# Kernel optimization log

Measured on AMD Instinct MI355X. Metric: run time of the kernel, lower is better.

The kernel has to match this reference:

```python
import jax, jax.numpy as jnp
import numpy as np

B_SZ = 8
D_MODEL = 512
D_STATE = 64
N2 = D_STATE // 2  # S4D uses complex-conjugate pairs -> d_state//2 complex modes
L_SEQ = 2048


def setup_inputs() -> dict:
    key = jax.random.key(0)
    ks = jax.random.split(key, 16)
    d = D_MODEL
    scale = 1.0 / np.sqrt(d)
    inp = {
        "x": jax.random.normal(ks[0], (B_SZ, d, L_SEQ), dtype=jnp.float32),
        # q/k/v projections (nn.Linear: weight (out,in), bias (out,))
        "Wq": jax.random.normal(ks[1], (d, d), dtype=jnp.float32) * scale,
        "bq": jax.random.normal(ks[2], (d,), dtype=jnp.float32) * scale,
        "Wk": jax.random.normal(ks[3], (d, d), dtype=jnp.float32) * scale,
        "bk": jax.random.normal(ks[4], (d,), dtype=jnp.float32) * scale,
        "Wv": jax.random.normal(ks[5], (d, d), dtype=jnp.float32) * scale,
        "bv": jax.random.normal(ks[6], (d,), dtype=jnp.float32) * scale,
        # Shift layer params
        "shift_C": jax.random.normal(ks[7], (1, d, D_STATE), dtype=jnp.float32),
        "shift_D": jax.random.normal(ks[8], (d,), dtype=jnp.float32),
        # S4D (diagonal SSM) params
        "log_dt": jax.random.uniform(ks[9], (d,), dtype=jnp.float32,
                                      minval=np.log(1e-3), maxval=np.log(1e-1)),
        "A_real": jnp.log(0.5 * jnp.ones((d, N2), dtype=jnp.float32)),
        "A_imag": jnp.broadcast_to(np.pi * jnp.arange(N2, dtype=jnp.float32), (d, N2)),
        "C_re": jax.random.normal(ks[10], (d, N2), dtype=jnp.float32) * np.sqrt(0.5),
        "C_im": jax.random.normal(ks[11], (d, N2), dtype=jnp.float32) * np.sqrt(0.5),
        "s4_D": jax.random.normal(ks[12], (d,), dtype=jnp.float32),
    }
    return inp


def _linear_chan(x, W, b):
    # x: (B, H, L); Linear applied over channel dim H -> (B, H_out, L)
    return jnp.einsum("bhl,dh->bdl", x, W) + b[:, None]


def _shift(u, C, Dp):
    """Shift SSM: causal conv with kernel = first L taps of C (computed via FFT
    exactly as the torch source does). u: (B, H, L)."""
    L = u.shape[-1]
    n = 2 * L
    H, S = C.shape[1], C.shape[2]
    Bmat = jnp.zeros((H, S), dtype=u.dtype).at[:, 0].set(1.0)
    B_fc = jnp.conj(jnp.fft.rfft(Bmat, n=n, axis=-1))  # (H, L+1)
    C_f = jnp.fft.rfft(C, n=n, axis=-1)                # (1, H, L+1)
    kernel = jnp.fft.irfft(B_fc * C_f, n=n, axis=-1)[..., :L]  # (1, H, L)
    kernel_f = jnp.fft.rfft(kernel, n=n, axis=-1)      # (1, H, L+1)
    u_f = jnp.fft.rfft(u, n=n, axis=-1)                # (B, H, L+1)
    y = jnp.fft.irfft(u_f * kernel_f, n=n, axis=-1)[..., :L]
    return y + u * Dp[:, None]


def _s4d(u, log_dt, A_real, A_imag, C_re, C_im, Dp):
    """Standard S4D forward: ZOH-discretized diagonal SSM kernel + FFT conv.
    u: (B, H, L)."""
    L = u.shape[-1]
    n = 2 * L
    dt = jnp.exp(log_dt)[:, None]                  # (H, 1)
    A = -jnp.exp(A_real) + 1j * A_imag             # (H, N2)
    dtA = A * dt                                   # (H, N2)
    C = (C_re + 1j * C_im) * (jnp.exp(dtA) - 1.0) / A
    vand = jnp.exp(dtA[:, :, None] * jnp.arange(L))  # (H, N2, L)
    K = 2.0 * jnp.einsum("hn,hnl->hl", C, vand).real  # (H, L)
    y = jnp.fft.irfft(jnp.fft.rfft(u, n=n, axis=-1) * jnp.fft.rfft(K, n=n, axis=-1),
                      n=n, axis=-1)[..., :L]
    return y + u * Dp[:, None]


def reference(x, Wq, bq, Wk, bk, Wv, bv, shift_C, shift_D,
              log_dt, A_real, A_imag, C_re, C_im, s4_D):
    q = _linear_chan(x, Wq, bq)
    k = _linear_chan(x, Wk, bk)
    v = _linear_chan(x, Wv, bv)
    shift_out = _shift(k, shift_C, shift_D)
    s4d_out = _s4d(v * shift_out, log_dt, A_real, A_imag, C_re, C_im, s4_D)
    return q * s4d_out
```

## Files before the change

### kernel.cpp

```cpp
#include <hip/hip_runtime.h>
#include <cstdint>


#define DMODEL 512
#define LSEQ 2048

typedef _Float16 half_t;
typedef __attribute__((ext_vector_type(4))) _Float16 half4v;
typedef __attribute__((ext_vector_type(8))) _Float16 half8v;
typedef __attribute__((ext_vector_type(4))) float floatx4;

#define SW(R, c) ((R) * 64 + ((((c) >> 3) ^ ((R) & 7)) << 3) + ((c) & 7))

__device__ __forceinline__ void gload_lds16(const half_t* g, half_t* l) {
  __builtin_amdgcn_global_load_lds(
      (const __attribute__((address_space(1))) uint32_t*)g,
      (__attribute__((address_space(3))) uint32_t*)l, 16, 0, 0);
}

#define WAIT_LGKM_BAR()                                   \
  do {                                                    \
    asm volatile("s_waitcnt lgkmcnt(0)" ::: "memory");    \
    __builtin_amdgcn_s_barrier();                         \
    __builtin_amdgcn_sched_barrier(0);                    \
  } while (0)

__global__ __launch_bounds__(256) void prep(
    const float* __restrict__ x, const float* __restrict__ Wq,
    const float* __restrict__ Wk, const float* __restrict__ Wv,
    const float* __restrict__ log_dt, const float* __restrict__ A_real,
    const float* __restrict__ A_imag, const float* __restrict__ C_re,
    const float* __restrict__ C_im, const float* __restrict__ shC,
    half_t* __restrict__ xT, half_t* __restrict__ W16,
    half_t* __restrict__ Vt, half_t* __restrict__ Et, half_t* __restrict__ Tt,
    half_t* __restrict__ T1t, half_t* __restrict__ T2t,
    float* __restrict__ wt2) {
  __shared__ float tile[64][68];
  __shared__ float aL[32], bL[32], wrL[32], wiL[32], crL[32], ciL[32];
  __shared__ float Kt[64], tapl[64];
  int bid = blockIdx.x;
  int tid = threadIdx.x;

  if (bid < 512) {
    int h = bid;
    if (tid < 64) { Kt[tid] = 0.f; tapl[tid] = shC[h * 64 + tid]; }
    if (tid < 32) {
      int n = tid, hn = h * 32 + n;
      float dt = expf(log_dt[h]);
      float Ar = -expf(A_real[hn]), Ai = A_imag[hn];
      float a = dt * Ar, b = dt * Ai;
      float ea = expf(a);
      float wr = ea * cosf(b), wi = ea * sinf(b);
      float Am2 = Ar * Ar + Ai * Ai;
      float zr = wr - 1.0f, zi = wi;
      float qr = (zr * Ar + zi * Ai) / Am2;
      float qi = (zi * Ar - zr * Ai) / Am2;
      aL[n] = a; bL[n] = b; wrL[n] = wr; wiL[n] = wi;
      crL[n] = C_re[hn] * qr - C_im[hn] * qi;
      ciL[n] = C_re[hn] * qi + C_im[hn] * qr;
      float e64 = expf(64.0f * a);
      wt2[h * 64 + 2 * n]     = e64 * cosf(64.0f * b);
      wt2[h * 64 + 2 * n + 1] = e64 * sinf(64.0f * b);
    }
    __syncthreads();
    size_t base = (size_t)h * 4096;
    {
      int r = tid >> 2;
      int nb = (tid & 3) * 8;
      float ksum = 0.f;
#pragma unroll
      for (int i = 0; i < 8; i++) {
        int n = nb + i;
        float a = aL[n], b = bL[n];
        float cr = crL[n], ci = ciL[n];
        float er = expf(a * (float)r);
        float w0r = er * cosf(b * (float)r), w0i = er * sinf(b * (float)r);
        ksum += 2.f * (cr * w0r - ci * w0i);
        float wr = wrL[n], wi = wiL[n];
        float w1r = w0r * wr - w0i * wi, w1i = w0r * wi + w0i * wr;
        Et[base + SW(r, 2 * n)]     = (half_t)(2.f * (cr * w1r - ci * w1i));
        Et[base + SW(r, 2 * n + 1)] = (half_t)(-2.f * (cr * w1i + ci * w1r));
        Vt[base + SW(2 * n, 63 - r)]     = (half_t)w0r;
        Vt[base + SW(2 * n + 1, 63 - r)] = (half_t)w0i;
      }
      atomicAdd(&Kt[r], ksum);
    }
    __syncthreads();
#pragma unroll
    for (int e = 0; e < 16; e++) {
      int idx = e * 256 + tid;
      int r = idx >> 6, t = idx & 63;
      int d = r - t;
      size_t a = base + SW(r, t);
      Tt[a]  = (d >= 0) ? (half_t)Kt[d] : (half_t)0.f;
      T1t[a] = (d >= 0) ? (half_t)tapl[d] : (half_t)0.f;
      T2t[a] = (d < 0) ? (half_t)tapl[64 + d] : (half_t)0.f;
    }
  } else if (bid < 2560) {
    int i = bid - 512;
    int b = i >> 8, rem = i & 255;
    int d0 = (rem >> 5) * 64, l0 = (rem & 31) * 64;
    int dy = tid >> 4, lx = tid & 15;
    const float* xp = x + ((size_t)(b * 512 + d0)) * 2048 + l0;
#pragma unroll
    for (int rr = 0; rr < 4; rr++) {
      float4 v = *(const float4*)(xp + (size_t)(rr * 16 + dy) * 2048 + lx * 4);
      *(float4*)&tile[rr * 16 + dy][lx * 4] = v;
    }
    __syncthreads();
    half_t* op = xT + ((size_t)(b * 2048 + l0)) * 512 + d0;
    int lr = tid >> 2, c4 = tid & 3;
#pragma unroll
    for (int cc = 0; cc < 2; cc++) {
      int ch = cc * 4 + c4;
      half8v hv;
#pragma unroll
      for (int e = 0; e < 8; e++) hv[e] = (half_t)tile[ch * 8 + e][lr];
      *(half8v*)(op + (size_t)lr * 512 + ch * 8) = hv;
    }
  } else {
    int base = (bid - 2560) * 256 + tid;
#pragma unroll
    for (int it = 0; it < 6; it++) {
      int i = base + it * 131072;
      const float* src = (i < 262144) ? Wq : ((i < 524288) ? Wk : Wv);
      W16[i] = (half_t)src[i & 262143];
    }
  }
}

__global__ __launch_bounds__(256) void gemm_qkv(
    const half_t* __restrict__ xT, const half_t* __restrict__ Wstk,
    const float* __restrict__ bq, const float* __restrict__ bk,
    const float* __restrict__ bv, half_t* __restrict__ outq,
    half_t* __restrict__ outk, half_t* __restrict__ outv) {
  __shared__ half_t smem[16384];
  half_t* As = smem;
  half_t* Bs = smem + 8192;
  int flat = blockIdx.x;
  int swz = (flat & 7) * 192 + (flat >> 3);
  int nt = swz / 12, mt = swz - nt * 12;
  int n0 = nt * 128, m0 = mt * 128;
  int tid = threadIdx.x;
  int lane = tid & 63, wid = tid >> 6;
  int wr = wid >> 1, wc = wid & 1;
  int lrow = lane & 15, lg = lane >> 4;
  int rsub = lane >> 3, ssub = lane & 7;
  int gslot = ssub ^ rsub;

  floatx4 acc[4][4];
#pragma unroll
  for (int i = 0; i < 4; i++)
#pragma unroll
    for (int j = 0; j < 4; j++) acc[i][j] = (floatx4){0.f, 0.f, 0.f, 0.f};

  const half_t* gA = Wstk + (size_t)(m0 + wid * 32 + rsub) * 512 + gslot * 8;
  const half_t* gB = xT + (size_t)(n0 + wid * 32 + rsub) * 512 + gslot * 8;

  for (int kk = 0; kk < 512; kk += 64) {
#pragma unroll
    for (int i = 0; i < 4; i++) {
      int c = wid * 4 + i;
      gload_lds16(gA + (size_t)i * 8 * 512 + kk, As + c * 512);
      gload_lds16(gB + (size_t)i * 8 * 512 + kk, Bs + c * 512);
    }
    __syncthreads();
#pragma unroll
    for (int h = 0; h < 2; h++) {
      half8v af[4], bf[4];
#pragma unroll
      for (int i = 0; i < 4; i++) {
        int r = wr * 64 + i * 16 + lrow;
        af[i] = *(const half8v*)(As + r * 64 + ((h * 4 + lg) ^ (r & 7)) * 8);
      }
#pragma unroll
      for (int j = 0; j < 4; j++) {
        int r = wc * 64 + j * 16 + lrow;
        bf[j] = *(const half8v*)(Bs + r * 64 + ((h * 4 + lg) ^ (r & 7)) * 8);
      }
#pragma unroll
      for (int i = 0; i < 4; i++)
#pragma unroll
        for (int j = 0; j < 4; j++)
          acc[i][j] = __builtin_amdgcn_mfma_f32_16x16x32_f16(af[i], bf[j],
                                                             acc[i][j], 0, 0, 0);
    }
    __syncthreads();
  }

  int z = m0 >> 9;
  const float* bias = (z == 0) ? bq : ((z == 1) ? bk : bv);
  half_t* smemC = smem;
#pragma unroll
  for (int i = 0; i < 4; i++) {
    int dl = wr * 64 + i * 16 + 4 * lg;
    float4 b4 = *(const float4*)&bias[(m0 + dl) & 511];
#pragma unroll
    for (int j = 0; j < 4; j++) {
      int ll = wc * 64 + j * 16 + lrow;
#pragma unroll
      for (int reg = 0; reg < 4; reg++) {
        int d = dl + reg;
        float val = acc[i][j][reg] + ((const float*)&b4)[reg];
        smemC[d * 128 + (((ll >> 3) ^ (d & 15)) << 3) + (ll & 7)] = (half_t)val;
      }
    }
  }
  __syncthreads();
  {
    int t4 = tid >> 4, ch = tid & 15;
    int b = n0 >> 11, l0 = n0 & 2047;
    half_t* outp = (z == 0) ? outq : ((z == 1) ? outk : outv);
#pragma unroll
    for (int rep = 0; rep < 8; rep++) {
      int d = rep * 16 + t4;
      half8v v = *(const half8v*)(smemC + d * 128 + ((ch ^ (d & 15)) << 3));
      size_t rowb = ((size_t)(b * 512 + ((m0 + d) & 511))) * 2048;
      if (z == 0) {
        *(half8v*)(outp + rowb + l0 + ch * 8) = v;
      } else {
        int j = (l0 >> 6) + (ch >> 3);
        int s = ch & 7;
        *(half8v*)(outp + rowb + j * 64 + ((s ^ (j & 7)) << 3)) = v;
      }
    }
  }
}

__global__ __launch_bounds__(256) void s4d_main(
    const half_t* __restrict__ kimg, const half_t* __restrict__ vimg,
    const half_t* __restrict__ T1t, const half_t* __restrict__ T2t,
    const half_t* __restrict__ Vt, const half_t* __restrict__ Et,
    const half_t* __restrict__ Tt, const float* __restrict__ wt2,
    const float* __restrict__ shD, const float* __restrict__ s4D,
    const half_t* __restrict__ qbuf, float* __restrict__ outp) {
  __shared__ half_t tabs[5][4096];
  __shared__ half_t kl[2][33 * 64];
  __shared__ half_t vg[2][32 * 64];
  __shared__ half_t uh[32 * 64];
  __shared__ float SG[32 * 66];
  int h = blockIdx.x;
  int tid = threadIdx.x;
  int lane = tid & 63, wid = tid >> 6;
  int lrow = lane & 15, lg = lane >> 4;
  int mi = wid & 1, ri0 = wid >> 1;

  {
    size_t tb = (size_t)h * 4096;
#pragma unroll
    for (int i = 0; i < 2; i++) {
      int c = wid * 2 + i;
      gload_lds16(T1t + tb + c * 512 + lane * 8, &tabs[0][c * 512]);
      gload_lds16(T2t + tb + c * 512 + lane * 8, &tabs[1][c * 512]);
      gload_lds16(Vt  + tb + c * 512 + lane * 8, &tabs[2][c * 512]);
      gload_lds16(Et  + tb + c * 512 + lane * 8, &tabs[3][c * 512]);
      gload_lds16(Tt  + tb + c * 512 + lane * 8, &tabs[4][c * 512]);
    }
    gload_lds16(kimg + (size_t)h * 2048 + wid * 512 + lane * 8,
                &kl[0][64 + wid * 512]);
    gload_lds16(vimg + (size_t)h * 2048 + wid * 512 + lane * 8,
                &vg[0][wid * 512]);
  }
  if (tid < 16) {
    half8v zz = {(_Float16)0, (_Float16)0, (_Float16)0, (_Float16)0,
                 (_Float16)0, (_Float16)0, (_Float16)0, (_Float16)0};
    *(half8v*)(&kl[tid >> 3][(tid & 7) * 8]) = zz;
  }
  float sDsh = shD[h];
  float sD4 = s4D[h];
  float wTr = wt2[h * 64 + 2 * (tid & 31)];
  float wTi = wt2[h * 64 + 2 * (tid & 31) + 1];
  const half_t* t1 = tabs[0];
  const half_t* t2 = tabs[1];
  const half_t* tV = tabs[2];
  const half_t* tE = tabs[3];
  const half_t* tT = tabs[4];

#define LDF(base, r, ks, key) \
  (*(const half8v*)((base) + (r) * 64 + (((ks) * 4 + lg) ^ (key)) * 8))

  int cur = 0;
  for (int bi = 0; bi < 8; bi++) {
    if (bi < 7) {
      size_t nb = (size_t)((bi + 1) * 512 + h) * 2048;
      gload_lds16(kimg + nb + wid * 512 + lane * 8, &kl[cur ^ 1][64 + wid * 512]);
      gload_lds16(vimg + nb + wid * 512 + lane * 8, &vg[cur ^ 1][wid * 512]);
      asm volatile("s_waitcnt vmcnt(2) lgkmcnt(0)" ::: "memory");
    } else {
      asm volatile("s_waitcnt vmcnt(0) lgkmcnt(0)" ::: "memory");
    }
    __builtin_amdgcn_s_barrier();
    __builtin_amdgcn_sched_barrier(0);

    const half_t* klc = kl[cur];
    half_t* vgc = vg[cur];
    floatx4 acc[2];

    acc[0] = (floatx4){0.f, 0.f, 0.f, 0.f};
    acc[1] = (floatx4){0.f, 0.f, 0.f, 0.f};
    {
      int jA = mi * 16 + lrow;
      int key1 = lrow & 7, key2 = (lrow + 7) & 7;
#pragma unroll
      for (int ks = 0; ks < 2; ks++) {
        half8v a1 = LDF(klc, 1 + jA, ks, key1);
        half8v a2 = LDF(klc, jA, ks, key2);
#pragma unroll
        for (int tt = 0; tt < 2; tt++) {
          int rb = (ri0 + tt * 2) * 16 + lrow;
          half8v b1 = LDF(t1, rb, ks, lrow & 7);
          half8v b2 = LDF(t2, rb, ks, lrow & 7);
          acc[tt] = __builtin_amdgcn_mfma_f32_16x16x32_f16(a1, b1, acc[tt], 0, 0, 0);
          acc[tt] = __builtin_amdgcn_mfma_f32_16x16x32_f16(a2, b2, acc[tt], 0, 0, 0);
        }
      }
    }
#pragma unroll
    for (int tt = 0; tt < 2; tt++) {
#pragma unroll
      for (int reg = 0; reg < 4; reg++) {
        int j = mi * 16 + 4 * lg + reg;
        int r = (ri0 + tt * 2) * 16 + lrow;
        int cph = (((r >> 3) ^ (j & 7)) << 3) + (r & 7);
        float kvv = (float)klc[(1 + j) * 64 + cph];
        float vvv = (float)vgc[j * 64 + cph];
        uh[j * 64 + cph] = (half_t)(vvv * (acc[tt][reg] + sDsh * kvv));
      }
    }
    WAIT_LGKM_BAR();

    acc[0] = (floatx4){0.f, 0.f, 0.f, 0.f};
    acc[1] = (floatx4){0.f, 0.f, 0.f, 0.f};
#pragma unroll
    for (int ks = 0; ks < 2; ks++) {
      half8v a = LDF(uh, mi * 16 + lrow, ks, lrow & 7);
#pragma unroll
      for (int tt = 0; tt < 2; tt++) {
        int rb = (ri0 + tt * 2) * 16 + lrow;
        half8v b = LDF(tV, rb, ks, lrow & 7);
        acc[tt] = __builtin_amdgcn_mfma_f32_16x16x32_f16(a, b, acc[tt], 0, 0, 0);
      }
    }
#pragma unroll
    for (int tt = 0; tt < 2; tt++) {
      int ri = ri0 + tt * 2;
#pragma unroll
      for (int reg = 0; reg < 4; reg++) {
        int j = mi * 16 + 4 * lg + reg;
        SG[j * 66 + ri * 16 + lrow] = acc[tt][reg];
      }
    }
    WAIT_LGKM_BAR();

    if (tid < 32) {
      int n = tid;
      float gr = 0.f, gi = 0.f;
      for (int j = 0; j < 32; j++) {
        float tr = SG[j * 66 + 2 * n], ti = SG[j * 66 + 2 * n + 1];
        SG[j * 66 + 2 * n] = gr; SG[j * 66 + 2 * n + 1] = gi;
        float nr = wTr * gr - wTi * gi + tr;
        gi = wTr * gi + wTi * gr + ti;
        gr = nr;
      }
    }
    WAIT_LGKM_BAR();

    {
      int j = tid >> 3, s = tid & 7;
      half8v g;
#pragma unroll
      for (int i = 0; i < 8; i++) g[i] = (half_t)SG[j * 66 + s * 8 + i];
      *(half8v*)(vgc + j * 64 + (s ^ (j & 7)) * 8) = g;
    }
    WAIT_LGKM_BAR();

    acc[0] = (floatx4){0.f, 0.f, 0.f, 0.f};
    acc[1] = (floatx4){0.f, 0.f, 0.f, 0.f};
#pragma unroll
    for (int ks = 0; ks < 2; ks++) {
      half8v ag = LDF(vgc, mi * 16 + lrow, ks, lrow & 7);
      half8v au = LDF(uh, mi * 16 + lrow, ks, lrow & 7);
#pragma unroll
      for (int tt = 0; tt < 2; tt++) {
        int rb = (ri0 + tt * 2) * 16 + lrow;
        half8v be = LDF(tE, rb, ks, lrow & 7);
        half8v bt = LDF(tT, rb, ks, lrow & 7);
        acc[tt] = __builtin_amdgcn_mfma_f32_16x16x32_f16(ag, be, acc[tt], 0, 0, 0);
        acc[tt] = __builtin_amdgcn_mfma_f32_16x16x32_f16(au, bt, acc[tt], 0, 0, 0);
      }
    }
#pragma unroll
    for (int tt = 0; tt < 2; tt++) {
#pragma unroll
      for (int reg = 0; reg < 4; reg++) {
        int j = mi * 16 + 4 * lg + reg;
        int r = (ri0 + tt * 2) * 16 + lrow;
        int cph = (((r >> 3) ^ (j & 7)) << 3) + (r & 7);
        SG[j * 64 + r] = acc[tt][reg] + sD4 * (float)uh[j * 64 + cph];
      }
    }
    WAIT_LGKM_BAR();

    {
      size_t bh = (size_t)(bi * 512 + h) * 2048;
      half8v qv = *(const half8v*)(qbuf + bh + tid * 8);
      float* op = outp + bh;
      float4 o0, o1;
      o0.x = (float)qv[0] * SG[tid * 8 + 0];
      o0.y = (float)qv[1] * SG[tid * 8 + 1];
      o0.z = (float)qv[2] * SG[tid * 8 + 2];
      o0.w = (float)qv[3] * SG[tid * 8 + 3];
      o1.x = (float)qv[4] * SG[tid * 8 + 4];
      o1.y = (float)qv[5] * SG[tid * 8 + 5];
      o1.z = (float)qv[6] * SG[tid * 8 + 6];
      o1.w = (float)qv[7] * SG[tid * 8 + 7];
      *(float4*)(op + tid * 8) = o0;
      *(float4*)(op + tid * 8 + 4) = o1;
    }
    WAIT_LGKM_BAR();
    cur ^= 1;
  }
#undef LDF
}

extern "C" void kernel_launch(void* const* d_in, const int* in_sizes, int n_in,
                              void* d_out, int out_size, void* d_ws, size_t ws_size,
                              hipStream_t stream) {
  const float* x      = (const float*)d_in[0];
  const float* Wq     = (const float*)d_in[1];
  const float* bq     = (const float*)d_in[2];
  const float* Wk     = (const float*)d_in[3];
  const float* bk     = (const float*)d_in[4];
  const float* Wv     = (const float*)d_in[5];
  const float* bv     = (const float*)d_in[6];
  const float* shC    = (const float*)d_in[7];
  const float* shD    = (const float*)d_in[8];
  const float* log_dt = (const float*)d_in[9];
  const float* A_real = (const float*)d_in[10];
  const float* A_imag = (const float*)d_in[11];
  const float* C_re   = (const float*)d_in[12];
  const float* C_im   = (const float*)d_in[13];
  const float* s4D    = (const float*)d_in[14];
  float* out = (float*)d_out;
  half_t* wsh = (half_t*)d_ws;

  half_t* qbuf = wsh;
  half_t* kbuf = wsh + 8388608;
  half_t* vbuf = wsh + 16777216;
  half_t* xT16 = wsh + 25165824;
  half_t* W16  = wsh + 33554432;
  half_t* Vt   = wsh + 34340864;
  half_t* Et   = wsh + 36438016;
  half_t* Tt   = wsh + 38535168;
  half_t* T1t  = wsh + 40632320;
  half_t* T2t  = wsh + 42729472;
  float*  wt2  = (float*)(wsh + 44826624);

  prep<<<3072, 256, 0, stream>>>(x, Wq, Wk, Wv, log_dt, A_real, A_imag,
                                 C_re, C_im, shC, xT16, W16,
                                 Vt, Et, Tt, T1t, T2t, wt2);
  gemm_qkv<<<dim3(1536), 256, 0, stream>>>(xT16, W16, bq, bk, bv,
                                           qbuf, kbuf, vbuf);
  s4d_main<<<512, 256, 0, stream>>>(kbuf, vbuf, T1t, T2t, Vt, Et, Tt,
                                    wt2, shD, s4D, qbuf, out);
}
```

Baseline: 86.13 us.

## Build SSM tables in s4d_main shared memory instead of global prep

Moves the per-channel table generation (Vandermonde, E, Toeplitz, shift taps, and the 64-step power) out of the prep kernel and into s4d_main, where the tables are written straight into LDS. This removes the global-memory round trip of five 4096-entry fp16 tables per channel and shrinks the prep grid. It also writes the scan carries directly as fp16 into the vg buffer, which drops one pass and one barrier, and removes the trailing barrier after the output store. In exchange, s4d_main does extra transcendental work before its main loop, and that work is no longer spread across the separate prep blocks.

```diff
diff --git a/kernel.cpp b/kernel.cpp
--- a/kernel.cpp
+++ b/kernel.cpp
@@ -6,6 +6,7 @@
 #define LSEQ 2048
 
 typedef _Float16 half_t;
+typedef __attribute__((ext_vector_type(2))) _Float16 half2v;
 typedef __attribute__((ext_vector_type(4))) _Float16 half4v;
 typedef __attribute__((ext_vector_type(8))) _Float16 half8v;
 typedef __attribute__((ext_vector_type(4))) float floatx4;
@@ -28,77 +29,12 @@
 __global__ __launch_bounds__(256) void prep(
     const float* __restrict__ x, const float* __restrict__ Wq,
     const float* __restrict__ Wk, const float* __restrict__ Wv,
-    const float* __restrict__ log_dt, const float* __restrict__ A_real,
-    const float* __restrict__ A_imag, const float* __restrict__ C_re,
-    const float* __restrict__ C_im, const float* __restrict__ shC,
-    half_t* __restrict__ xT, half_t* __restrict__ W16,
-    half_t* __restrict__ Vt, half_t* __restrict__ Et, half_t* __restrict__ Tt,
-    half_t* __restrict__ T1t, half_t* __restrict__ T2t,
-    float* __restrict__ wt2) {
+    half_t* __restrict__ xT, half_t* __restrict__ W16) {
   __shared__ float tile[64][68];
-  __shared__ float aL[32], bL[32], wrL[32], wiL[32], crL[32], ciL[32];
-  __shared__ float Kt[64], tapl[64];
   int bid = blockIdx.x;
   int tid = threadIdx.x;
-
-  if (bid < 512) {
-    int h = bid;
-    if (tid < 64) { Kt[tid] = 0.f; tapl[tid] = shC[h * 64 + tid]; }
-    if (tid < 32) {
-      int n = tid, hn = h * 32 + n;
-      float dt = expf(log_dt[h]);
-      float Ar = -expf(A_real[hn]), Ai = A_imag[hn];
-      float a = dt * Ar, b = dt * Ai;
-      float ea = expf(a);
-      float wr = ea * cosf(b), wi = ea * sinf(b);
-      float Am2 = Ar * Ar + Ai * Ai;
-      float zr = wr - 1.0f, zi = wi;
-      float qr = (zr * Ar + zi * Ai) / Am2;
-      float qi = (zi * Ar - zr * Ai) / Am2;
-      aL[n] = a; bL[n] = b; wrL[n] = wr; wiL[n] = wi;
-      crL[n] = C_re[hn] * qr - C_im[hn] * qi;
-      ciL[n] = C_re[hn] * qi + C_im[hn] * qr;
-      float e64 = expf(64.0f * a);
-      wt2[h * 64 + 2 * n]     = e64 * cosf(64.0f * b);
-      wt2[h * 64 + 2 * n + 1] = e64 * sinf(64.0f * b);
-    }
-    __syncthreads();
-    size_t base = (size_t)h * 4096;
-    {
-      int r = tid >> 2;
-      int nb = (tid & 3) * 8;
-      float ksum = 0.f;
-#pragma unroll
-      for (int i = 0; i < 8; i++) {
-        int n = nb + i;
-        float a = aL[n], b = bL[n];
-        float cr = crL[n], ci = ciL[n];
-        float er = expf(a * (float)r);
-        float w0r = er * cosf(b * (float)r), w0i = er * sinf(b * (float)r);
-        ksum += 2.f * (cr * w0r - ci * w0i);
-        float wr = wrL[n], wi = wiL[n];
-        float w1r = w0r * wr - w0i * wi, w1i = w0r * wi + w0i * wr;
-        Et[base + SW(r, 2 * n)]     = (half_t)(2.f * (cr * w1r - ci * w1i));
-        Et[base + SW(r, 2 * n + 1)] = (half_t)(-2.f * (cr * w1i + ci * w1r));
-        Vt[base + SW(2 * n, 63 - r)]     = (half_t)w0r;
-        Vt[base + SW(2 * n + 1, 63 - r)] = (half_t)w0i;
-      }
-      atomicAdd(&Kt[r], ksum);
-    }
-    __syncthreads();
-#pragma unroll
-    for (int e = 0; e < 16; e++) {
-      int idx = e * 256 + tid;
-      int r = idx >> 6, t = idx & 63;
-      int d = r - t;
-      size_t a = base + SW(r, t);
-      Tt[a]  = (d >= 0) ? (half_t)Kt[d] : (half_t)0.f;
-      T1t[a] = (d >= 0) ? (half_t)tapl[d] : (half_t)0.f;
-      T2t[a] = (d < 0) ? (half_t)tapl[64 + d] : (half_t)0.f;
-    }
-  } else if (bid < 2560) {
-    int i = bid - 512;
-    int b = i >> 8, rem = i & 255;
+  if (bid < 2048) {
+    int b = bid >> 8, rem = bid & 255;
     int d0 = (rem >> 5) * 64, l0 = (rem & 31) * 64;
     int dy = tid >> 4, lx = tid & 15;
     const float* xp = x + ((size_t)(b * 512 + d0)) * 2048 + l0;
@@ -119,7 +55,7 @@
       *(half8v*)(op + (size_t)lr * 512 + ch * 8) = hv;
     }
   } else {
-    int base = (bid - 2560) * 256 + tid;
+    int base = (bid - 2048) * 256 + tid;
 #pragma unroll
     for (int it = 0; it < 6; it++) {
       int i = base + it * 131072;
@@ -229,9 +165,9 @@
 
 __global__ __launch_bounds__(256) void s4d_main(
     const half_t* __restrict__ kimg, const half_t* __restrict__ vimg,
-    const half_t* __restrict__ T1t, const half_t* __restrict__ T2t,
-    const half_t* __restrict__ Vt, const half_t* __restrict__ Et,
-    const half_t* __restrict__ Tt, const float* __restrict__ wt2,
+    const float* __restrict__ shC, const float* __restrict__ log_dt,
+    const float* __restrict__ A_real, const float* __restrict__ A_imag,
+    const float* __restrict__ C_re, const float* __restrict__ C_im,
     const float* __restrict__ shD, const float* __restrict__ s4D,
     const half_t* __restrict__ qbuf, float* __restrict__ outp) {
   __shared__ half_t tabs[5][4096];
@@ -245,31 +181,82 @@
   int lrow = lane & 15, lg = lane >> 4;
   int mi = wid & 1, ri0 = wid >> 1;
 
-  {
-    size_t tb = (size_t)h * 4096;
-#pragma unroll
-    for (int i = 0; i < 2; i++) {
-      int c = wid * 2 + i;
-      gload_lds16(T1t + tb + c * 512 + lane * 8, &tabs[0][c * 512]);
-      gload_lds16(T2t + tb + c * 512 + lane * 8, &tabs[1][c * 512]);
-      gload_lds16(Vt  + tb + c * 512 + lane * 8, &tabs[2][c * 512]);
-      gload_lds16(Et  + tb + c * 512 + lane * 8, &tabs[3][c * 512]);
-      gload_lds16(Tt  + tb + c * 512 + lane * 8, &tabs[4][c * 512]);
-    }
-    gload_lds16(kimg + (size_t)h * 2048 + wid * 512 + lane * 8,
-                &kl[0][64 + wid * 512]);
-    gload_lds16(vimg + (size_t)h * 2048 + wid * 512 + lane * 8,
-                &vg[0][wid * 512]);
-  }
+  gload_lds16(kimg + (size_t)h * 2048 + wid * 512 + lane * 8,
+              &kl[0][64 + wid * 512]);
+  gload_lds16(vimg + (size_t)h * 2048 + wid * 512 + lane * 8,
+              &vg[0][wid * 512]);
   if (tid < 16) {
     half8v zz = {(_Float16)0, (_Float16)0, (_Float16)0, (_Float16)0,
                  (_Float16)0, (_Float16)0, (_Float16)0, (_Float16)0};
     *(half8v*)(&kl[tid >> 3][(tid & 7) * 8]) = zz;
   }
+
+  float* Kt   = SG;
+  float* tapl = SG + 64;
+  float* aL   = SG + 128;
+  float* bL   = SG + 160;
+  float* wrL  = SG + 192;
+  float* wiL  = SG + 224;
+  float* crL  = SG + 256;
+  float* ciL  = SG + 288;
+  if (tid < 64) { Kt[tid] = 0.f; tapl[tid] = shC[h * 64 + tid]; }
+  if (tid < 32) {
+    int n = tid, hn = h * 32 + n;
+    float dt = expf(log_dt[h]);
+    float Ar = -expf(A_real[hn]), Ai = A_imag[hn];
+    float a = dt * Ar, b = dt * Ai;
+    float ea = expf(a);
+    float wr = ea * cosf(b), wi = ea * sinf(b);
+    float Am2 = Ar * Ar + Ai * Ai;
+    float zr = wr - 1.0f, zi = wi;
+    float qr = (zr * Ar + zi * Ai) / Am2;
+    float qi = (zi * Ar - zr * Ai) / Am2;
+    aL[n] = a; bL[n] = b; wrL[n] = wr; wiL[n] = wi;
+    crL[n] = C_re[hn] * qr - C_im[hn] * qi;
+    ciL[n] = C_re[hn] * qi + C_im[hn] * qr;
+  }
+  __syncthreads();
+  float wTr, wTi;
+  {
+    int n = tid & 31;
+    float e64 = expf(64.f * aL[n]);
+    float b64 = 64.f * bL[n];
+    wTr = e64 * cosf(b64);
+    wTi = e64 * sinf(b64);
+  }
+  {
+    int r = tid >> 2, nb = (tid & 3) * 8;
+    float ksum = 0.f;
+#pragma unroll
+    for (int i = 0; i < 8; i++) {
+      int n = nb + i;
+      float a = aL[n], b = bL[n];
+      float cr = crL[n], ci = ciL[n];
+      float er = expf(a * (float)r);
+      float w0r = er * cosf(b * (float)r), w0i = er * sinf(b * (float)r);
+      ksum += 2.f * (cr * w0r - ci * w0i);
+      float wr = wrL[n], wi = wiL[n];
+      float w1r = w0r * wr - w0i * wi, w1i = w0r * wi + w0i * wr;
+      tabs[3][SW(r, 2 * n)]     = (half_t)(2.f * (cr * w1r - ci * w1i));
+      tabs[3][SW(r, 2 * n + 1)] = (half_t)(-2.f * (cr * w1i + ci * w1r));
+      tabs[2][SW(2 * n, 63 - r)]     = (half_t)w0r;
+      tabs[2][SW(2 * n + 1, 63 - r)] = (half_t)w0i;
+    }
+    atomicAdd(&Kt[r], ksum);
+  }
+  __syncthreads();
+#pragma unroll
+  for (int e = 0; e < 16; e++) {
+    int idx = e * 256 + tid;
+    int r = idx >> 6, t = idx & 63;
+    int d = r - t;
+    int a = SW(r, t);
+    tabs[4][a] = (d >= 0) ? (half_t)Kt[d] : (half_t)0.f;
+    tabs[0][a] = (d >= 0) ? (half_t)tapl[d] : (half_t)0.f;
+    tabs[1][a] = (d < 0) ? (half_t)tapl[64 + d] : (half_t)0.f;
+  }
   float sDsh = shD[h];
   float sD4 = s4D[h];
-  float wTr = wt2[h * 64 + 2 * (tid & 31)];
-  float wTi = wt2[h * 64 + 2 * (tid & 31) + 1];
   const half_t* t1 = tabs[0];
   const half_t* t2 = tabs[1];
   const half_t* tV = tabs[2];
@@ -355,22 +342,15 @@
     if (tid < 32) {
       int n = tid;
       float gr = 0.f, gi = 0.f;
+#pragma unroll 4
       for (int j = 0; j < 32; j++) {
         float tr = SG[j * 66 + 2 * n], ti = SG[j * 66 + 2 * n + 1];
-        SG[j * 66 + 2 * n] = gr; SG[j * 66 + 2 * n + 1] = gi;
+        half2v gp = {(half_t)gr, (half_t)gi};
+        *(half2v*)(vgc + j * 64 + (((n >> 2) ^ (j & 7)) << 3) + 2 * (n & 3)) = gp;
         float nr = wTr * gr - wTi * gi + tr;
         gi = wTr * gi + wTi * gr + ti;
         gr = nr;
       }
-    }
-    WAIT_LGKM_BAR();
-
-    {
-      int j = tid >> 3, s = tid & 7;
-      half8v g;
-#pragma unroll
-      for (int i = 0; i < 8; i++) g[i] = (half_t)SG[j * 66 + s * 8 + i];
-      *(half8v*)(vgc + j * 64 + (s ^ (j & 7)) * 8) = g;
     }
     WAIT_LGKM_BAR();
 
@@ -417,7 +397,6 @@
       *(float4*)(op + tid * 8) = o0;
       *(float4*)(op + tid * 8 + 4) = o1;
     }
-    WAIT_LGKM_BAR();
     cur ^= 1;
   }
 #undef LDF
@@ -449,18 +428,10 @@
   half_t* vbuf = wsh + 16777216;
   half_t* xT16 = wsh + 25165824;
   half_t* W16  = wsh + 33554432;
-  half_t* Vt   = wsh + 34340864;
-  half_t* Et   = wsh + 36438016;
-  half_t* Tt   = wsh + 38535168;
-  half_t* T1t  = wsh + 40632320;
-  half_t* T2t  = wsh + 42729472;
-  float*  wt2  = (float*)(wsh + 44826624);
-
-  prep<<<3072, 256, 0, stream>>>(x, Wq, Wk, Wv, log_dt, A_real, A_imag,
-                                 C_re, C_im, shC, xT16, W16,
-                                 Vt, Et, Tt, T1t, T2t, wt2);
+
+  prep<<<2560, 256, 0, stream>>>(x, Wq, Wk, Wv, xT16, W16);
   gemm_qkv<<<dim3(1536), 256, 0, stream>>>(xT16, W16, bq, bk, bv,
                                            qbuf, kbuf, vbuf);
-  s4d_main<<<512, 256, 0, stream>>>(kbuf, vbuf, T1t, T2t, Vt, Et, Tt,
-                                    wt2, shD, s4D, qbuf, out);
+  s4d_main<<<512, 256, 0, stream>>>(kbuf, vbuf, shC, log_dt, A_real, A_imag,
+                                    C_re, C_im, shD, s4D, qbuf, out);
 }
```

Result: no change. 84.75 us, median of 2 (-1.6%).

## Split s4d_main into one block per (batch, channel) with reduced LDS footprint

Applied to the files above, without the earlier changes.

Changes s4d_main from 512 blocks that each loop over all 8 batches to 4096 blocks that each handle one (batch, channel) pair, using a swizzled block index so blocks sharing a channel's tables are close in launch order. LDS use is cut: a single kl/vg buffer and three table slots, with the E/T tables loaded into slots after T1/T2 are consumed, overlapping that load with the V-table GEMM. The scan now writes half-precision results straight into the swizzled vg layout, removing one barrier pass. The aim is more occupancy and parallelism. The cost is re-loading each channel's 40KB of tables once per batch instead of once per channel.

```diff
diff --git a/kernel.cpp b/kernel.cpp
--- a/kernel.cpp
+++ b/kernel.cpp
@@ -6,6 +6,7 @@
 #define LSEQ 2048
 
 typedef _Float16 half_t;
+typedef __attribute__((ext_vector_type(2))) _Float16 half2v;
 typedef __attribute__((ext_vector_type(4))) _Float16 half4v;
 typedef __attribute__((ext_vector_type(8))) _Float16 half8v;
 typedef __attribute__((ext_vector_type(4))) float floatx4;
@@ -234,12 +235,16 @@
     const half_t* __restrict__ Tt, const float* __restrict__ wt2,
     const float* __restrict__ shD, const float* __restrict__ s4D,
     const half_t* __restrict__ qbuf, float* __restrict__ outp) {
-  __shared__ half_t tabs[5][4096];
-  __shared__ half_t kl[2][33 * 64];
-  __shared__ half_t vg[2][32 * 64];
+  __shared__ half_t kl[33 * 64];
+  __shared__ half_t vg[32 * 64];
   __shared__ half_t uh[32 * 64];
+  __shared__ half_t tabA[4096];
+  __shared__ half_t tabB[4096];
+  __shared__ half_t tabC[4096];
   __shared__ float SG[32 * 66];
-  int h = blockIdx.x;
+  int swz = (blockIdx.x & 7) * 512 + (blockIdx.x >> 3);
+  int h = swz >> 3, bi = swz & 7;
+  int bh = bi * 512 + h;
   int tid = threadIdx.x;
   int lane = tid & 63, wid = tid >> 6;
   int lrow = lane & 15, lg = lane >> 4;
@@ -247,178 +252,160 @@
 
   {
     size_t tb = (size_t)h * 4096;
+    gload_lds16(kimg + (size_t)bh * 2048 + wid * 512 + lane * 8,
+                kl + 64 + wid * 512);
+    gload_lds16(vimg + (size_t)bh * 2048 + wid * 512 + lane * 8,
+                vg + wid * 512);
 #pragma unroll
     for (int i = 0; i < 2; i++) {
       int c = wid * 2 + i;
-      gload_lds16(T1t + tb + c * 512 + lane * 8, &tabs[0][c * 512]);
-      gload_lds16(T2t + tb + c * 512 + lane * 8, &tabs[1][c * 512]);
-      gload_lds16(Vt  + tb + c * 512 + lane * 8, &tabs[2][c * 512]);
-      gload_lds16(Et  + tb + c * 512 + lane * 8, &tabs[3][c * 512]);
-      gload_lds16(Tt  + tb + c * 512 + lane * 8, &tabs[4][c * 512]);
-    }
-    gload_lds16(kimg + (size_t)h * 2048 + wid * 512 + lane * 8,
-                &kl[0][64 + wid * 512]);
-    gload_lds16(vimg + (size_t)h * 2048 + wid * 512 + lane * 8,
-                &vg[0][wid * 512]);
-  }
-  if (tid < 16) {
+      gload_lds16(T1t + tb + c * 512 + lane * 8, tabA + c * 512);
+      gload_lds16(T2t + tb + c * 512 + lane * 8, tabB + c * 512);
+      gload_lds16(Vt + tb + c * 512 + lane * 8, tabC + c * 512);
+    }
+  }
+  if (tid < 8) {
     half8v zz = {(_Float16)0, (_Float16)0, (_Float16)0, (_Float16)0,
                  (_Float16)0, (_Float16)0, (_Float16)0, (_Float16)0};
-    *(half8v*)(&kl[tid >> 3][(tid & 7) * 8]) = zz;
+    *(half8v*)(kl + tid * 8) = zz;
   }
   float sDsh = shD[h];
   float sD4 = s4D[h];
   float wTr = wt2[h * 64 + 2 * (tid & 31)];
   float wTi = wt2[h * 64 + 2 * (tid & 31) + 1];
-  const half_t* t1 = tabs[0];
-  const half_t* t2 = tabs[1];
-  const half_t* tV = tabs[2];
-  const half_t* tE = tabs[3];
-  const half_t* tT = tabs[4];
+  asm volatile("s_waitcnt vmcnt(0) lgkmcnt(0)" ::: "memory");
+  __builtin_amdgcn_s_barrier();
+  __builtin_amdgcn_sched_barrier(0);
 
 #define LDF(base, r, ks, key) \
   (*(const half8v*)((base) + (r) * 64 + (((ks) * 4 + lg) ^ (key)) * 8))
 
-  int cur = 0;
-  for (int bi = 0; bi < 8; bi++) {
-    if (bi < 7) {
-      size_t nb = (size_t)((bi + 1) * 512 + h) * 2048;
-      gload_lds16(kimg + nb + wid * 512 + lane * 8, &kl[cur ^ 1][64 + wid * 512]);
-      gload_lds16(vimg + nb + wid * 512 + lane * 8, &vg[cur ^ 1][wid * 512]);
-      asm volatile("s_waitcnt vmcnt(2) lgkmcnt(0)" ::: "memory");
-    } else {
-      asm volatile("s_waitcnt vmcnt(0) lgkmcnt(0)" ::: "memory");
-    }
-    __builtin_amdgcn_s_barrier();
-    __builtin_amdgcn_sched_barrier(0);
-
-    const half_t* klc = kl[cur];
-    half_t* vgc = vg[cur];
-    floatx4 acc[2];
-
-    acc[0] = (floatx4){0.f, 0.f, 0.f, 0.f};
-    acc[1] = (floatx4){0.f, 0.f, 0.f, 0.f};
-    {
-      int jA = mi * 16 + lrow;
-      int key1 = lrow & 7, key2 = (lrow + 7) & 7;
-#pragma unroll
-      for (int ks = 0; ks < 2; ks++) {
-        half8v a1 = LDF(klc, 1 + jA, ks, key1);
-        half8v a2 = LDF(klc, jA, ks, key2);
-#pragma unroll
-        for (int tt = 0; tt < 2; tt++) {
-          int rb = (ri0 + tt * 2) * 16 + lrow;
-          half8v b1 = LDF(t1, rb, ks, lrow & 7);
-          half8v b2 = LDF(t2, rb, ks, lrow & 7);
-          acc[tt] = __builtin_amdgcn_mfma_f32_16x16x32_f16(a1, b1, acc[tt], 0, 0, 0);
-          acc[tt] = __builtin_amdgcn_mfma_f32_16x16x32_f16(a2, b2, acc[tt], 0, 0, 0);
-        }
-      }
-    }
-#pragma unroll
-    for (int tt = 0; tt < 2; tt++) {
-#pragma unroll
-      for (int reg = 0; reg < 4; reg++) {
-        int j = mi * 16 + 4 * lg + reg;
-        int r = (ri0 + tt * 2) * 16 + lrow;
-        int cph = (((r >> 3) ^ (j & 7)) << 3) + (r & 7);
-        float kvv = (float)klc[(1 + j) * 64 + cph];
-        float vvv = (float)vgc[j * 64 + cph];
-        uh[j * 64 + cph] = (half_t)(vvv * (acc[tt][reg] + sDsh * kvv));
-      }
-    }
-    WAIT_LGKM_BAR();
-
-    acc[0] = (floatx4){0.f, 0.f, 0.f, 0.f};
-    acc[1] = (floatx4){0.f, 0.f, 0.f, 0.f};
+  floatx4 acc[2];
+  acc[0] = (floatx4){0.f, 0.f, 0.f, 0.f};
+  acc[1] = (floatx4){0.f, 0.f, 0.f, 0.f};
+  {
+    int jA = mi * 16 + lrow;
+    int key1 = lrow & 7, key2 = (lrow + 7) & 7;
 #pragma unroll
     for (int ks = 0; ks < 2; ks++) {
-      half8v a = LDF(uh, mi * 16 + lrow, ks, lrow & 7);
+      half8v a1 = LDF(kl, 1 + jA, ks, key1);
+      half8v a2 = LDF(kl, jA, ks, key2);
 #pragma unroll
       for (int tt = 0; tt < 2; tt++) {
         int rb = (ri0 + tt * 2) * 16 + lrow;
-        half8v b = LDF(tV, rb, ks, lrow & 7);
-        acc[tt] = __builtin_amdgcn_mfma_f32_16x16x32_f16(a, b, acc[tt], 0, 0, 0);
-      }
-    }
+        half8v b1 = LDF(tabA, rb, ks, lrow & 7);
+        half8v b2 = LDF(tabB, rb, ks, lrow & 7);
+        acc[tt] = __builtin_amdgcn_mfma_f32_16x16x32_f16(a1, b1, acc[tt], 0, 0, 0);
+        acc[tt] = __builtin_amdgcn_mfma_f32_16x16x32_f16(a2, b2, acc[tt], 0, 0, 0);
+      }
+    }
+  }
+#pragma unroll
+  for (int tt = 0; tt < 2; tt++) {
+#pragma unroll
+    for (int reg = 0; reg < 4; reg++) {
+      int j = mi * 16 + 4 * lg + reg;
+      int r = (ri0 + tt * 2) * 16 + lrow;
+      int cph = (((r >> 3) ^ (j & 7)) << 3) + (r & 7);
+      float kvv = (float)kl[(1 + j) * 64 + cph];
+      float vvv = (float)vg[j * 64 + cph];
+      uh[j * 64 + cph] = (half_t)(vvv * (acc[tt][reg] + sDsh * kvv));
+    }
+  }
+  WAIT_LGKM_BAR();
+
+  {
+    size_t tb = (size_t)h * 4096;
+#pragma unroll
+    for (int i = 0; i < 2; i++) {
+      int c = wid * 2 + i;
+      gload_lds16(Et + tb + c * 512 + lane * 8, tabA + c * 512);
+      gload_lds16(Tt + tb + c * 512 + lane * 8, tabB + c * 512);
+    }
+  }
+
+  acc[0] = (floatx4){0.f, 0.f, 0.f, 0.f};
+  acc[1] = (floatx4){0.f, 0.f, 0.f, 0.f};
+#pragma unroll
+  for (int ks = 0; ks < 2; ks++) {
+    half8v a = LDF(uh, mi * 16 + lrow, ks, lrow & 7);
 #pragma unroll
     for (int tt = 0; tt < 2; tt++) {
-      int ri = ri0 + tt * 2;
-#pragma unroll
-      for (int reg = 0; reg < 4; reg++) {
-        int j = mi * 16 + 4 * lg + reg;
-        SG[j * 66 + ri * 16 + lrow] = acc[tt][reg];
-      }
-    }
-    WAIT_LGKM_BAR();
-
-    if (tid < 32) {
-      int n = tid;
-      float gr = 0.f, gi = 0.f;
-      for (int j = 0; j < 32; j++) {
-        float tr = SG[j * 66 + 2 * n], ti = SG[j * 66 + 2 * n + 1];
-        SG[j * 66 + 2 * n] = gr; SG[j * 66 + 2 * n + 1] = gi;
-        float nr = wTr * gr - wTi * gi + tr;
-        gi = wTr * gi + wTi * gr + ti;
-        gr = nr;
-      }
-    }
-    WAIT_LGKM_BAR();
-
-    {
-      int j = tid >> 3, s = tid & 7;
-      half8v g;
-#pragma unroll
-      for (int i = 0; i < 8; i++) g[i] = (half_t)SG[j * 66 + s * 8 + i];
-      *(half8v*)(vgc + j * 64 + (s ^ (j & 7)) * 8) = g;
-    }
-    WAIT_LGKM_BAR();
-
-    acc[0] = (floatx4){0.f, 0.f, 0.f, 0.f};
-    acc[1] = (floatx4){0.f, 0.f, 0.f, 0.f};
-#pragma unroll
-    for (int ks = 0; ks < 2; ks++) {
-      half8v ag = LDF(vgc, mi * 16 + lrow, ks, lrow & 7);
-      half8v au = LDF(uh, mi * 16 + lrow, ks, lrow & 7);
-#pragma unroll
-      for (int tt = 0; tt < 2; tt++) {
-        int rb = (ri0 + tt * 2) * 16 + lrow;
-        half8v be = LDF(tE, rb, ks, lrow & 7);
-        half8v bt = LDF(tT, rb, ks, lrow & 7);
-        acc[tt] = __builtin_amdgcn_mfma_f32_16x16x32_f16(ag, be, acc[tt], 0, 0, 0);
-        acc[tt] = __builtin_amdgcn_mfma_f32_16x16x32_f16(au, bt, acc[tt], 0, 0, 0);
-      }
-    }
+      int rb = (ri0 + tt * 2) * 16 + lrow;
+      half8v b = LDF(tabC, rb, ks, lrow & 7);
+      acc[tt] = __builtin_amdgcn_mfma_f32_16x16x32_f16(a, b, acc[tt], 0, 0, 0);
+    }
+  }
+#pragma unroll
+  for (int tt = 0; tt < 2; tt++) {
+    int ri = ri0 + tt * 2;
+#pragma unroll
+    for (int reg = 0; reg < 4; reg++) {
+      int j = mi * 16 + 4 * lg + reg;
+      SG[j * 66 + ri * 16 + lrow] = acc[tt][reg];
+    }
+  }
+  asm volatile("s_waitcnt vmcnt(0) lgkmcnt(0)" ::: "memory");
+  __builtin_amdgcn_s_barrier();
+  __builtin_amdgcn_sched_barrier(0);
+
+  if (tid < 32) {
+    int n = tid;
+    float gr = 0.f, gi = 0.f;
+#pragma unroll 4
+    for (int j = 0; j < 32; j++) {
+      float tr = SG[j * 66 + 2 * n], ti = SG[j * 66 + 2 * n + 1];
+      half2v gp = {(half_t)gr, (half_t)gi};
+      *(half2v*)(vg + j * 64 + (((n >> 2) ^ (j & 7)) << 3) + 2 * (n & 3)) = gp;
+      float nr = wTr * gr - wTi * gi + tr;
+      gi = wTr * gi + wTi * gr + ti;
+      gr = nr;
+    }
+  }
+  WAIT_LGKM_BAR();
+
+  acc[0] = (floatx4){0.f, 0.f, 0.f, 0.f};
+  acc[1] = (floatx4){0.f, 0.f, 0.f, 0.f};
+#pragma unroll
+  for (int ks = 0; ks < 2; ks++) {
+    half8v ag = LDF(vg, mi * 16 + lrow, ks, lrow & 7);
+    half8v au = LDF(uh, mi * 16 + lrow, ks, lrow & 7);
 #pragma unroll
     for (int tt = 0; tt < 2; tt++) {
-#pragma unroll
-      for (int reg = 0; reg < 4; reg++) {
-        int j = mi * 16 + 4 * lg + reg;
-        int r = (ri0 + tt * 2) * 16 + lrow;
-        int cph = (((r >> 3) ^ (j & 7)) << 3) + (r & 7);
-        SG[j * 64 + r] = acc[tt][reg] + sD4 * (float)uh[j * 64 + cph];
-      }
-    }
-    WAIT_LGKM_BAR();
-
-    {
-      size_t bh = (size_t)(bi * 512 + h) * 2048;
-      half8v qv = *(const half8v*)(qbuf + bh + tid * 8);
-      float* op = outp + bh;
-      float4 o0, o1;
-      o0.x = (float)qv[0] * SG[tid * 8 + 0];
-      o0.y = (float)qv[1] * SG[tid * 8 + 1];
-      o0.z = (float)qv[2] * SG[tid * 8 + 2];
-      o0.w = (float)qv[3] * SG[tid * 8 + 3];
-      o1.x = (float)qv[4] * SG[tid * 8 + 4];
-      o1.y = (float)qv[5] * SG[tid * 8 + 5];
-      o1.z = (float)qv[6] * SG[tid * 8 + 6];
-      o1.w = (float)qv[7] * SG[tid * 8 + 7];
-      *(float4*)(op + tid * 8) = o0;
-      *(float4*)(op + tid * 8 + 4) = o1;
-    }
-    WAIT_LGKM_BAR();
-    cur ^= 1;
+      int rb = (ri0 + tt * 2) * 16 + lrow;
+      half8v be = LDF(tabA, rb, ks, lrow & 7);
+      half8v bt = LDF(tabB, rb, ks, lrow & 7);
+      acc[tt] = __builtin_amdgcn_mfma_f32_16x16x32_f16(ag, be, acc[tt], 0, 0, 0);
+      acc[tt] = __builtin_amdgcn_mfma_f32_16x16x32_f16(au, bt, acc[tt], 0, 0, 0);
+    }
+  }
+#pragma unroll
+  for (int tt = 0; tt < 2; tt++) {
+#pragma unroll
+    for (int reg = 0; reg < 4; reg++) {
+      int j = mi * 16 + 4 * lg + reg;
+      int r = (ri0 + tt * 2) * 16 + lrow;
+      int cph = (((r >> 3) ^ (j & 7)) << 3) + (r & 7);
+      SG[j * 64 + r] = acc[tt][reg] + sD4 * (float)uh[j * 64 + cph];
+    }
+  }
+  WAIT_LGKM_BAR();
+
+  {
+    size_t base = (size_t)bh * 2048;
+    half8v qv = *(const half8v*)(qbuf + base + tid * 8);
+    float* op = outp + base;
+    float4 o0, o1;
+    o0.x = (float)qv[0] * SG[tid * 8 + 0];
+    o0.y = (float)qv[1] * SG[tid * 8 + 1];
+    o0.z = (float)qv[2] * SG[tid * 8 + 2];
+    o0.w = (float)qv[3] * SG[tid * 8 + 3];
+    o1.x = (float)qv[4] * SG[tid * 8 + 4];
+    o1.y = (float)qv[5] * SG[tid * 8 + 5];
+    o1.z = (float)qv[6] * SG[tid * 8 + 6];
+    o1.w = (float)qv[7] * SG[tid * 8 + 7];
+    *(float4*)(op + tid * 8) = o0;
+    *(float4*)(op + tid * 8 + 4) = o1;
   }
 #undef LDF
 }
@@ -461,6 +448,6 @@
                                  Vt, Et, Tt, T1t, T2t, wt2);
   gemm_qkv<<<dim3(1536), 256, 0, stream>>>(xT16, W16, bq, bk, bv,
                                            qbuf, kbuf, vbuf);
-  s4d_main<<<512, 256, 0, stream>>>(kbuf, vbuf, T1t, T2t, Vt, Et, Tt,
-                                    wt2, shD, s4D, qbuf, out);
+  s4d_main<<<4096, 256, 0, stream>>>(kbuf, vbuf, T1t, T2t, Vt, Et, Tt,
+                                     wt2, shD, s4D, qbuf, out);
 }
```

Measured after the change: 85.38 us. Within noise of the previous version (-0.9%).
